# Kernel optimization log

Hardware: AMD Instinct MI355X
Metric: run time of the kernel (lower is better)

Reference implementation:

```python
import jax, jax.numpy as jnp
import numpy as np

B, S, V, D, H, C, NH = 8, 512, 32000, 768, 768, 9, 8
DH = D // NH


def setup_inputs() -> dict:
    key = jax.random.key(0)
    ks = list(jax.random.split(key, 24))
    it = iter(ks)

    def w(shape, s=0.02):
        return jax.random.normal(next(it), shape, jnp.float32) * s

    return {
        "input_ids": jax.random.randint(next(it), (B, S), 0, V, dtype=jnp.int32),
        "labels": jax.random.randint(next(it), (B, S), 0, C, dtype=jnp.int32),
        "emb_table": w((V, D), 1.0),
        "hw_Wh": w((D, D)),
        "hw_bh": jnp.zeros((D,), jnp.float32),
        "hw_Wt": w((D, D)),
        "hw_bt": jnp.zeros((D,), jnp.float32),
        "in_proj_w": w((3 * D, D)),
        "in_proj_b": jnp.zeros((3 * D,), jnp.float32),
        "out_proj_w": w((D, D)),
        "out_proj_b": jnp.zeros((D,), jnp.float32),
        "lstm0_Wih": w((2, 4 * H, D)),
        "lstm0_Whh": w((2, 4 * H, H)),
        "lstm0_b": jnp.zeros((2, 4 * H), jnp.float32),
        "lstm1_Wih": w((2, 4 * H, 2 * H)),
        "lstm1_Whh": w((2, 4 * H, H)),
        "lstm1_b": jnp.zeros((2, 4 * H), jnp.float32),
        "fc_W": w((C, 2 * H)),
        "fc_b": jnp.zeros((C,), jnp.float32),
        "crf_start": w((C,), 0.1),
        "crf_end": w((C,), 0.1),
        "crf_trans": w((C, C), 0.1),
    }


def _lstm_dir(x, Wih, Whh, b, reverse):
    # x: [B,S,in] -> outputs [B,S,H]; PyTorch gate order i,f,g,o
    xt = x.transpose(1, 0, 2)  # [S,B,in]
    h0 = jnp.zeros((x.shape[0], H), x.dtype)

    def step(carry, xt_):
        h, c = carry
        g = xt_ @ Wih.T + h @ Whh.T + b
        i, f, gg, o = jnp.split(g, 4, axis=-1)
        c = jax.nn.sigmoid(f) * c + jax.nn.sigmoid(i) * jnp.tanh(gg)
        h = jax.nn.sigmoid(o) * jnp.tanh(c)
        return (h, c), h

    _, hs = jax.lax.scan(step, (h0, h0), xt, reverse=reverse)
    return hs.transpose(1, 0, 2)


def _bilstm_layer(x, Wih, Whh, b):
    fwd = _lstm_dir(x, Wih[0], Whh[0], b[0], False)
    bwd = _lstm_dir(x, Wih[1], Whh[1], b[1], True)
    return jnp.concatenate([fwd, bwd], axis=-1)


def _emissions(input_ids, emb_table, hw_Wh, hw_bh, hw_Wt, hw_bt,
               in_proj_w, in_proj_b, out_proj_w, out_proj_b,
               lstm0_Wih, lstm0_Whh, lstm0_b, lstm1_Wih, lstm1_Whh, lstm1_b,
               fc_W, fc_b):
    x = emb_table[input_ids]  # [B,S,D]
    # Highway (1 layer, relu)
    hh = jax.nn.relu(x @ hw_Wh.T + hw_bh)
    t = jax.nn.sigmoid(x @ hw_Wt.T + hw_bt)
    x = t * hh + (1.0 - t) * x
    # Multi-head self-attention
    qkv = x @ in_proj_w.T + in_proj_b
    q, k, v = jnp.split(qkv, 3, axis=-1)
    hd = lambda a: a.reshape(B, S, NH, DH).transpose(0, 2, 1, 3)  # [B,NH,S,DH]
    q, k, v = hd(q), hd(k), hd(v)
    att = jax.nn.softmax(jnp.einsum('bhqd,bhkd->bhqk', q, k) / np.float32(np.sqrt(DH)), axis=-1)
    o = jnp.einsum('bhqk,bhkd->bhqd', att, v).transpose(0, 2, 1, 3).reshape(B, S, D)
    x = o @ out_proj_w.T + out_proj_b
    # 2-layer BiLSTM (inference: dropout off)
    x = _bilstm_layer(x, lstm0_Wih, lstm0_Whh, lstm0_b)
    x = _bilstm_layer(x, lstm1_Wih, lstm1_Whh, lstm1_b)
    return x @ fc_W.T + fc_b  # [B,S,C]


def _crf_nll(emissions, tags, crf_start, crf_end, crf_trans):
    # full mask (labels==-100 replaced by 0 before mask built), reduction='sum'
    em_t = emissions.transpose(1, 0, 2)  # [S,B,C]
    num = crf_start[tags[:, 0]] + crf_end[tags[:, -1]]
    num = num + jnp.take_along_axis(emissions, tags[..., None], axis=-1)[..., 0].sum(-1)
    num = num + crf_trans[tags[:, :-1], tags[:, 1:]].sum(-1)
    a0 = crf_start + em_t[0]  # [B,C]

    def fstep(a, em):
        a = jax.scipy.special.logsumexp(a[:, :, None] + crf_trans[None], axis=1) + em
        return a, None

    aT, _ = jax.lax.scan(fstep, a0, em_t[1:])
    logZ = jax.scipy.special.logsumexp(aT + crf_end, axis=-1)
    return -(num - logZ).sum()


def _viterbi(emissions, crf_start, crf_end, crf_trans):
    em_t = emissions.transpose(1, 0, 2)  # [S,B,C]
    s0 = crf_start + em_t[0]

    def vstep(s, em):
        sc = s[:, :, None] + crf_trans[None]  # [B,C_prev,C_next]
        return jnp.max(sc, axis=1) + em, jnp.argmax(sc, axis=1)

    sT, bps = jax.lax.scan(vstep, s0, em_t[1:])  # bps: [S-1,B,C]
    last = jnp.argmax(sT + crf_end, axis=-1)  # [B]

    def bstep(tag, bp):
        prev = jnp.take_along_axis(bp, tag[:, None], axis=1)[:, 0]
        return prev, prev

    _, path = jax.lax.scan(bstep, last, bps, reverse=True)  # [S-1,B]
    return jnp.concatenate([path, last[None]], axis=0).transpose(1, 0)  # [B,S]


def reference(input_ids, labels, emb_table, hw_Wh, hw_bh, hw_Wt, hw_bt,
              in_proj_w, in_proj_b, out_proj_w, out_proj_b,
              lstm0_Wih, lstm0_Whh, lstm0_b, lstm1_Wih, lstm1_Whh, lstm1_b,
              fc_W, fc_b, crf_start, crf_end, crf_trans):
    emissions = _emissions(input_ids, emb_table, hw_Wh, hw_bh, hw_Wt, hw_bt,
                           in_proj_w, in_proj_b, out_proj_w, out_proj_b,
                           lstm0_Wih, lstm0_Whh, lstm0_b,
                           lstm1_Wih, lstm1_Whh, lstm1_b, fc_W, fc_b)
    loss = _crf_nll(emissions, labels, crf_start, crf_end, crf_trans)
    decode = _viterbi(emissions, crf_start, crf_end, crf_trans)
    return loss, decode
```

## Files before the change

kernel.cpp:

```cpp
#include <hip/hip_runtime.h>
#include <cstdint>

#define B_   8
#define S_   512
#define D_   768
#define C_   9
#define BS_  4096

typedef unsigned long long u64;

__global__ __launch_bounds__(192) void k_embed(const int* __restrict__ ids,
                                               const float* __restrict__ emb,
                                               float* __restrict__ x) {
  int row = blockIdx.x;
  int id = ids[row];
  const float4* src = (const float4*)(emb + (size_t)id * D_);
  float4* dst = (float4*)(x + (size_t)row * D_);
  dst[threadIdx.x] = src[threadIdx.x];
}

#define GIDX(k, m) ((k)*144 + (m) + (((m) >> 5) << 2))

__global__ __launch_bounds__(256) void k_gemm(const float* __restrict__ A,
                                              const float* __restrict__ W,
                                              const float* __restrict__ bias,
                                              float* __restrict__ C,
                                              int M, int N, int K, int act, int mode) {
  __shared__ float As[2304];
  __shared__ float Bs[2304];
  int bm0 = blockIdx.y * 128, bn0 = blockIdx.x * 128;
  int tid = threadIdx.x;
  int tm = tid >> 4, tn = tid & 15;
  float acc[8][8];
#pragma unroll
  for (int i = 0; i < 8; ++i)
#pragma unroll
    for (int j = 0; j < 8; ++j) acc[i][j] = 0.f;

  for (int k0 = 0; k0 < K; k0 += 16) {
    __syncthreads();
#pragma unroll
    for (int j = 0; j < 2; ++j) {
      int f4 = tid + j * 256;
      int r = f4 >> 2;
      int kq = (f4 & 3) * 4;
      float4 va = *(const float4*)(A + (size_t)(bm0 + r) * K + k0 + kq);
      As[GIDX(kq + 0, r)] = va.x; As[GIDX(kq + 1, r)] = va.y;
      As[GIDX(kq + 2, r)] = va.z; As[GIDX(kq + 3, r)] = va.w;
      float4 vb = *(const float4*)(W + (size_t)(bn0 + r) * K + k0 + kq);
      Bs[GIDX(kq + 0, r)] = vb.x; Bs[GIDX(kq + 1, r)] = vb.y;
      Bs[GIDX(kq + 2, r)] = vb.z; Bs[GIDX(kq + 3, r)] = vb.w;
    }
    __syncthreads();
#pragma unroll
    for (int kk = 0; kk < 16; ++kk) {
      float a[8], b[8];
      *(float4*)&a[0] = *(const float4*)&As[GIDX(kk, tm * 8)];
      *(float4*)&a[4] = *(const float4*)&As[GIDX(kk, tm * 8 + 4)];
      *(float4*)&b[0] = *(const float4*)&Bs[GIDX(kk, tn * 8)];
      *(float4*)&b[4] = *(const float4*)&Bs[GIDX(kk, tn * 8 + 4)];
#pragma unroll
      for (int i = 0; i < 8; ++i)
#pragma unroll
        for (int j = 0; j < 8; ++j) acc[i][j] += a[i] * b[j];
    }
  }

  float bv[8];
#pragma unroll
  for (int j = 0; j < 8; ++j) bv[j] = bias[bn0 + tn * 8 + j];
#pragma unroll
  for (int i = 0; i < 8; ++i) {
    int row = bm0 + tm * 8 + i;
    float o[8];
#pragma unroll
    for (int j = 0; j < 8; ++j) {
      float v = acc[i][j] + bv[j];
      if (act == 1) v = fmaxf(v, 0.f);
      else if (act == 2) v = 1.f / (1.f + expf(-v));
      o[j] = v;
    }
    if (mode == 0) {
      float* cp = C + (size_t)row * N + bn0 + tn * 8;
      *(float4*)cp = make_float4(o[0], o[1], o[2], o[3]);
      *(float4*)(cp + 4) = make_float4(o[4], o[5], o[6], o[7]);
    } else {
      int bb = row >> 9, t = row & 511;
#pragma unroll
      for (int j = 0; j < 8; ++j) {
        unsigned n = bn0 + tn * 8 + j;
        unsigned dir = n / 3072u;
        unsigned n2 = n - dir * 3072u;
        unsigned g = n2 / 768u;
        unsigned rem = n2 - g * 768u;
        unsigned grp = rem >> 3, u = rem & 7;
        C[(((size_t)(dir * 512 + t) * 96 + grp) << 8) + u * 32 + g * 8 + bb] = o[j];
      }
    }
  }
}

__global__ __launch_bounds__(256) void k_highway(float* __restrict__ x,
                                                 const float* __restrict__ hh,
                                                 const float* __restrict__ tt) {
  const int n4 = BS_ * D_ / 4;
  for (int i = blockIdx.x * 256 + threadIdx.x; i < n4; i += gridDim.x * 256) {
    float4 xv = ((const float4*)x)[i];
    float4 hv = ((const float4*)hh)[i];
    float4 tv = ((const float4*)tt)[i];
    xv.x = tv.x * hv.x + (1.f - tv.x) * xv.x;
    xv.y = tv.y * hv.y + (1.f - tv.y) * xv.y;
    xv.z = tv.z * hv.z + (1.f - tv.z) * xv.z;
    xv.w = tv.w * hv.w + (1.f - tv.w) * xv.w;
    ((float4*)x)[i] = xv;
  }
}

__global__ __launch_bounds__(256) void k_attn(const float* __restrict__ qkv,
                                              float* __restrict__ out) {
  __shared__ float Qs[16 * 100];
  __shared__ float Ks[32 * 101];
  __shared__ float Ps[16 * 513];
  int bh = blockIdx.x;
  int b = bh >> 3, h = bh & 7;
  int q0 = blockIdx.y * 16;
  int tid = threadIdx.x;
  const float scale = 0.10206207261596577f;

  const float* qb = qkv + (size_t)(b * 512 + q0) * 2304 + h * 96;
  for (int i = tid; i < 16 * 96; i += 256) {
    int r = i / 96, c = i - r * 96;
    Qs[r * 100 + c] = qb[(size_t)r * 2304 + c];
  }
  int qi = tid >> 4, kseg = tid & 15;

  for (int kt = 0; kt < 16; ++kt) {
    __syncthreads();
    const float* kb = qkv + (size_t)(b * 512 + kt * 32) * 2304 + 768 + h * 96;
    for (int i = tid; i < 32 * 96; i += 256) {
      int r = i / 96, c = i - r * 96;
      Ks[r * 101 + c] = kb[(size_t)r * 2304 + c];
    }
    __syncthreads();
    int kj0 = kseg * 2;
    float s0 = 0.f, s1 = 0.f;
    const float* qrow = &Qs[qi * 100];
    const float* k0p = &Ks[kj0 * 101];
    const float* k1p = &Ks[(kj0 + 1) * 101];
#pragma unroll 8
    for (int d = 0; d < 96; ++d) {
      float qv = qrow[d];
      s0 += qv * k0p[d];
      s1 += qv * k1p[d];
    }
    Ps[qi * 513 + kt * 32 + kj0] = s0 * scale;
    Ps[qi * 513 + kt * 32 + kj0 + 1] = s1 * scale;
  }
  __syncthreads();

  {
    float m = -1e30f;
    for (int j = 0; j < 32; ++j) m = fmaxf(m, Ps[qi * 513 + kseg + j * 16]);
    m = fmaxf(m, __shfl_xor(m, 1)); m = fmaxf(m, __shfl_xor(m, 2));
    m = fmaxf(m, __shfl_xor(m, 4)); m = fmaxf(m, __shfl_xor(m, 8));
    float sum = 0.f;
    for (int j = 0; j < 32; ++j) {
      int idx = qi * 513 + kseg + j * 16;
      float e = expf(Ps[idx] - m);
      Ps[idx] = e;
      sum += e;
    }
    sum += __shfl_xor(sum, 1); sum += __shfl_xor(sum, 2);
    sum += __shfl_xor(sum, 4); sum += __shfl_xor(sum, 8);
    float inv = 1.f / sum;
    for (int j = 0; j < 32; ++j) Ps[qi * 513 + kseg + j * 16] *= inv;
  }

  float acc[6] = {0.f, 0.f, 0.f, 0.f, 0.f, 0.f};
  int d0 = kseg * 6;
  for (int kt = 0; kt < 16; ++kt) {
    __syncthreads();
    const float* vb = qkv + (size_t)(b * 512 + kt * 32) * 2304 + 1536 + h * 96;
    for (int i = tid; i < 32 * 96; i += 256) {
      int r = i / 96, c = i - r * 96;
      Ks[r * 101 + c] = vb[(size_t)r * 2304 + c];
    }
    __syncthreads();
#pragma unroll 4
    for (int kj = 0; kj < 32; ++kj) {
      float p = Ps[qi * 513 + kt * 32 + kj];
      const float* vrow = &Ks[kj * 101 + d0];
#pragma unroll
      for (int u = 0; u < 6; ++u) acc[u] += p * vrow[u];
    }
  }
  float* ob = out + (size_t)(b * 512 + q0 + qi) * 768 + h * 96 + d0;
#pragma unroll
  for (int u = 0; u < 6; ++u) ob[u] = acc[u];
}

#define NWGD 96
__global__ __launch_bounds__(256, 1) void k_lstm(const float* __restrict__ gates,
                                                 const float* __restrict__ Whh,
                                                 float* __restrict__ hbuf,
                                                 float* __restrict__ hs,
                                                 int* __restrict__ flags) {
  __shared__ float hlds[8 * 772];
  int tid = threadIdx.x;
  int wg = blockIdx.x;
  int dir = wg / NWGD;
  int grp = wg % NWGD;
  int rg = tid >> 5;
  int ks = tid & 31;

  float4 w4[4][6];
#pragma unroll
  for (int j = 0; j < 4; ++j) {
    const float* wp = Whh + ((size_t)dir * 3072 + j * 768 + grp * 8 + rg) * 768 + ks * 4;
#pragma unroll
    for (int jj = 0; jj < 6; ++jj)
      w4[j][jj] = *(const float4*)(wp + jj * 128);
  }

  float* hb = hbuf + (size_t)dir * 2 * 6144;
  const float* gbase = gates + (size_t)dir * 512 * 24576 + grp * 256 + tid;
  int* barp = flags;
  float cst = 0.f;
  const float* hp = hlds + ks * 4;

  for (int step = 0; step < 512; ++step) {
    int t = dir ? (511 - step) : step;
    float gqv = gbase[(size_t)t * 24576];

#pragma unroll
    for (int i = 0; i < 3; ++i) {
      int idx = i * 256 + tid;
      int b2 = idx / 96;
      int kq = (idx - b2 * 96) * 8;
      const u64* src = (const u64*)(hb + (step & 1) * 6144 + b2 * 768 + kq);
      u64 lo = __hip_atomic_load(src + 0, __ATOMIC_RELAXED, __HIP_MEMORY_SCOPE_AGENT);
      u64 hi = __hip_atomic_load(src + 1, __ATOMIC_RELAXED, __HIP_MEMORY_SCOPE_AGENT);
      u64 lo2 = __hip_atomic_load(src + 2, __ATOMIC_RELAXED, __HIP_MEMORY_SCOPE_AGENT);
      u64 hi2 = __hip_atomic_load(src + 3, __ATOMIC_RELAXED, __HIP_MEMORY_SCOPE_AGENT);
      float* dst = &hlds[b2 * 772 + kq];
      *(u64*)(dst + 0) = lo;
      *(u64*)(dst + 2) = hi;
      *(u64*)(dst + 4) = lo2;
      *(u64*)(dst + 6) = hi2;
    }
    __syncthreads();

    float v[32];
#pragma unroll
    for (int i = 0; i < 32; ++i) v[i] = 0.f;
#pragma unroll
    for (int jj = 0; jj < 6; ++jj) {
#pragma unroll
      for (int b2 = 0; b2 < 8; ++b2) {
        float4 hv = *(const float4*)(hp + b2 * 772 + jj * 128);
#pragma unroll
        for (int j = 0; j < 4; ++j) {
          float4 w = w4[j][jj];
          v[j * 8 + b2] = fmaf(w.x, hv.x, v[j * 8 + b2]);
          v[j * 8 + b2] = fmaf(w.y, hv.y, v[j * 8 + b2]);
          v[j * 8 + b2] = fmaf(w.z, hv.z, v[j * 8 + b2]);
          v[j * 8 + b2] = fmaf(w.w, hv.w, v[j * 8 + b2]);
        }
      }
    }

    {
      bool hi = (ks & 16) != 0;
#pragma unroll
      for (int i = 0; i < 16; ++i) {
        float keep = hi ? v[i + 16] : v[i];
        float send = hi ? v[i] : v[i + 16];
        v[i] = keep + __shfl_xor(send, 16);
      }
    }
    {
      bool hi = (ks & 8) != 0;
#pragma unroll
      for (int i = 0; i < 8; ++i) {
        float keep = hi ? v[i + 8] : v[i];
        float send = hi ? v[i] : v[i + 8];
        v[i] = keep + __shfl_xor(send, 8);
      }
    }
    {
      bool hi = (ks & 4) != 0;
#pragma unroll
      for (int i = 0; i < 4; ++i) {
        float keep = hi ? v[i + 4] : v[i];
        float send = hi ? v[i] : v[i + 4];
        v[i] = keep + __shfl_xor(send, 4);
      }
    }
    {
      bool hi = (ks & 2) != 0;
#pragma unroll
      for (int i = 0; i < 2; ++i) {
        float keep = hi ? v[i + 2] : v[i];
        float send = hi ? v[i] : v[i + 2];
        v[i] = keep + __shfl_xor(send, 2);
      }
    }
    {
      bool hi = (ks & 1) != 0;
      float keep = hi ? v[1] : v[0];
      float send = hi ? v[0] : v[1];
      v[0] = keep + __shfl_xor(send, 1);
    }

    float gv = v[0] + gqv;
    float gf = __shfl_down(gv, 8);
    float gg = __shfl_down(gv, 16);
    float go = __shfl_down(gv, 24);
    if (ks < 8) {
      float i_ = 1.f / (1.f + expf(-gv));
      float f_ = 1.f / (1.f + expf(-gf));
      float ci = tanhf(gg);
      float o_ = 1.f / (1.f + expf(-go));
      cst = f_ * cst + i_ * ci;
      float hnew = o_ * tanhf(cst);
      int hidden = grp * 8 + rg;
      __hip_atomic_store(hb + ((step + 1) & 1) * 6144 + ks * 768 + hidden, hnew,
                         __ATOMIC_RELAXED, __HIP_MEMORY_SCOPE_AGENT);
      hs[((size_t)(ks * 512 + t)) * 1536 + dir * 768 + hidden] = hnew;
    }

    __syncthreads();
    if (tid == 0)
      __hip_atomic_store(&barp[wg * 32], step + 1, __ATOMIC_RELAXED, __HIP_MEMORY_SCOPE_AGENT);
    if (tid < NWGD) {
      const int* fp = &barp[(dir * NWGD + tid) * 32];
      while (__hip_atomic_load(fp, __ATOMIC_RELAXED, __HIP_MEMORY_SCOPE_AGENT) <= step)
        __builtin_amdgcn_s_sleep(2);
    }
    __syncthreads();
  }
}

__global__ __launch_bounds__(256) void k_fc(const float* __restrict__ A,
                                            const float* __restrict__ Wf,
                                            const float* __restrict__ bf,
                                            float* __restrict__ out) {
  __shared__ float Wl[9 * 1536];
  int tid = threadIdx.x;
  for (int i = tid; i < 9 * 1536; i += 256) Wl[i] = Wf[i];
  __syncthreads();
  int lane = tid & 63, wv = tid >> 6;
  int row = blockIdx.x * 4 + wv;
  const float* a = A + (size_t)row * 1536;
  float acc[9];
#pragma unroll
  for (int c = 0; c < 9; ++c) acc[c] = 0.f;
  for (int i = 0; i < 24; ++i) {
    float av = a[lane + i * 64];
#pragma unroll
    for (int c = 0; c < 9; ++c) acc[c] += av * Wl[c * 1536 + lane + i * 64];
  }
#pragma unroll
  for (int c = 0; c < 9; ++c) {
#pragma unroll
    for (int m = 1; m < 64; m <<= 1) acc[c] += __shfl_xor(acc[c], m);
  }
  if (lane == 0) {
#pragma unroll
    for (int c = 0; c < 9; ++c) out[(size_t)row * 9 + c] = acc[c] + bf[c];
  }
}

__global__ __launch_bounds__(128) void k_crf(const float* __restrict__ em,
                                             const int* __restrict__ labels,
                                             const float* __restrict__ cs,
                                             const float* __restrict__ ce,
                                             const float* __restrict__ ct,
                                             float* __restrict__ out) {
  __shared__ float trans[9][12];
  __shared__ float ab[2][8][9];
  __shared__ float vb[2][8][9];
  __shared__ unsigned char bps[511][8][9];
  __shared__ float red[128];
  __shared__ float lz[8];
  int tid = threadIdx.x;
  if (tid < 81) trans[tid / 9][tid % 9] = ct[tid];
  if (tid < 72) {
    int b = tid / 9, c = tid % 9;
    float v = cs[c] + em[(b * 512) * 9 + c];
    ab[0][b][c] = v;
    vb[0][b][c] = v;
  }
  __syncthreads();
  for (int t = 1; t < 512; ++t) {
    int rp = (t - 1) & 1, wp = t & 1;
    if (tid < 72) {
      int b = tid / 9, cn = tid % 9;
      float e = em[(b * 512 + t) * 9 + cn];
      float m = -1e30f, vm = -1e30f;
      int bp = 0;
#pragma unroll
      for (int cp = 0; cp < 9; ++cp) {
        float x = ab[rp][b][cp] + trans[cp][cn];
        m = fmaxf(m, x);
        float y = vb[rp][b][cp] + trans[cp][cn];
        if (y > vm) { vm = y; bp = cp; }
      }
      float ssum = 0.f;
#pragma unroll
      for (int cp = 0; cp < 9; ++cp)
        ssum += expf(ab[rp][b][cp] + trans[cp][cn] - m);
      ab[wp][b][cn] = m + logf(ssum) + e;
      vb[wp][b][cn] = vm + e;
      bps[t - 1][b][cn] = (unsigned char)bp;
    }
    __syncthreads();
  }
  float part = 0.f;
  for (int idx = tid; idx < 4096; idx += 128) {
    int b = idx >> 9, t = idx & 511;
    int tg = labels[b * 512 + t];
    part += em[(b * 512 + t) * 9 + tg];
    if (t < 511) part += trans[tg][labels[b * 512 + t + 1]];
  }
  if (tid < 8) part += cs[labels[tid * 512]] + ce[labels[tid * 512 + 511]];
  red[tid] = part;
  __syncthreads();
  for (int s2 = 64; s2 > 0; s2 >>= 1) {
    if (tid < s2) red[tid] += red[tid + s2];
    __syncthreads();
  }
  if (tid < 8) {
    int b = tid;
    float m = -1e30f;
#pragma unroll
    for (int c = 0; c < 9; ++c) m = fmaxf(m, ab[1][b][c] + ce[c]);
    float ssum = 0.f;
#pragma unroll
    for (int c = 0; c < 9; ++c) ssum += expf(ab[1][b][c] + ce[c] - m);
    lz[b] = m + logf(ssum);
  }
  __syncthreads();
  if (tid == 0) {
    float z = 0.f;
#pragma unroll
    for (int b = 0; b < 8; ++b) z += lz[b];
    out[0] = -(red[0] - z);
  }
  if (tid < 8) {
    int b = tid;
    float bv2 = vb[1][b][0] + ce[0];
    int best = 0;
#pragma unroll
    for (int c = 1; c < 9; ++c) {
      float y = vb[1][b][c] + ce[c];
      if (y > bv2) { bv2 = y; best = c; }
    }
    out[1 + b * 512 + 511] = (float)best;
    int tg = best;
    for (int t = 510; t >= 0; --t) {
      tg = bps[t][b][tg];
      out[1 + b * 512 + t] = (float)tg;
    }
  }
}

extern "C" void kernel_launch(void* const* d_in, const int* in_sizes, int n_in,
                              void* d_out, int out_size, void* d_ws, size_t ws_size,
                              hipStream_t stream) {
  (void)in_sizes; (void)n_in; (void)out_size; (void)ws_size;
  const int*   ids    = (const int*)d_in[0];
  const int*   labels = (const int*)d_in[1];
  const float* emb    = (const float*)d_in[2];
  const float* hwWh   = (const float*)d_in[3];
  const float* hwbh   = (const float*)d_in[4];
  const float* hwWt   = (const float*)d_in[5];
  const float* hwbt   = (const float*)d_in[6];
  const float* ipw    = (const float*)d_in[7];
  const float* ipb    = (const float*)d_in[8];
  const float* opw    = (const float*)d_in[9];
  const float* opb    = (const float*)d_in[10];
  const float* l0Wih  = (const float*)d_in[11];
  const float* l0Whh  = (const float*)d_in[12];
  const float* l0b    = (const float*)d_in[13];
  const float* l1Wih  = (const float*)d_in[14];
  const float* l1Whh  = (const float*)d_in[15];
  const float* l1b    = (const float*)d_in[16];
  const float* fcW    = (const float*)d_in[17];
  const float* fcb    = (const float*)d_in[18];
  const float* cs     = (const float*)d_in[19];
  const float* ce     = (const float*)d_in[20];
  const float* ct     = (const float*)d_in[21];

  float* ws   = (float*)d_ws;
  float* x0   = ws;
  float* gbuf = ws + 3145728;
  float* hh   = gbuf;
  float* tt   = gbuf + 3145728;
  float* qkv  = gbuf + 6291456;
  float* x1   = ws + 28311552;
  float* hs0  = ws + 31457280;
  float* hs1  = ws + 37748736;
  float* em   = ws + 44040192;
  float* hbuf = ws + 44077056;
  int*   flags = (int*)(ws + 44101632);

  dim3 g768(6, 32), g2304(18, 32), g6144(48, 32);

  k_embed<<<BS_, 192, 0, stream>>>(ids, emb, x0);
  k_gemm<<<g768, 256, 0, stream>>>(x0, hwWh, hwbh, hh, BS_, 768, 768, 1, 0);
  k_gemm<<<g768, 256, 0, stream>>>(x0, hwWt, hwbt, tt, BS_, 768, 768, 2, 0);
  k_highway<<<768, 256, 0, stream>>>(x0, hh, tt);
  k_gemm<<<g2304, 256, 0, stream>>>(x0, ipw, ipb, qkv, BS_, 2304, 768, 0, 0);
  k_attn<<<dim3(64, 32), 256, 0, stream>>>(qkv, x0);
  k_gemm<<<g768, 256, 0, stream>>>(x0, opw, opb, x1, BS_, 768, 768, 0, 0);

  k_gemm<<<g6144, 256, 0, stream>>>(x1, l0Wih, l0b, gbuf, BS_, 6144, 768, 0, 1);
  hipMemsetAsync(hbuf, 0, (24576 + 192 * 32) * sizeof(float), stream);
  k_lstm<<<192, 256, 0, stream>>>(gbuf, l0Whh, hbuf, hs0, flags);

  k_gemm<<<g6144, 256, 0, stream>>>(hs0, l1Wih, l1b, gbuf, BS_, 6144, 1536, 0, 1);
  hipMemsetAsync(hbuf, 0, (24576 + 192 * 32) * sizeof(float), stream);
  k_lstm<<<192, 256, 0, stream>>>(gbuf, l1Whh, hbuf, hs1, flags);

  k_fc<<<1024, 256, 0, stream>>>(hs1, fcW, fcb, em);
  k_crf<<<1, 128, 0, stream>>>(em, labels, cs, ce, ct, (float*)d_out);
}
```

Baseline: 8.109 ms.

## Double-buffer GEMM smem, defer LSTM hs store, wave-per-batch CRF

The GEMM now uses double-buffered shared memory, with the next K-tile loaded into registers while the current one is computed, which removes one barrier per iteration. The LSTM step moves the global hs write after the barrier flag store so it leaves the critical path. The CRF kernel is rewritten to use one wavefront per batch, exchanging values with shuffles instead of a block-wide sync every timestep, and it prefetches emissions. The cost is more shared memory and registers in the GEMM, and a different CRF reduction order.

```diff
diff --git a/kernel.cpp b/kernel.cpp
--- a/kernel.cpp
+++ b/kernel.cpp
@@ -26,43 +26,69 @@
                                               const float* __restrict__ bias,
                                               float* __restrict__ C,
                                               int M, int N, int K, int act, int mode) {
-  __shared__ float As[2304];
-  __shared__ float Bs[2304];
+  __shared__ float As[2][2304];
+  __shared__ float Bs[2][2304];
   int bm0 = blockIdx.y * 128, bn0 = blockIdx.x * 128;
   int tid = threadIdx.x;
   int tm = tid >> 4, tn = tid & 15;
+  int r0 = tid >> 2, kq = (tid & 3) * 4;
+  const float* Aptr = A + (size_t)(bm0 + r0) * K + kq;
+  const float* Wptr = W + (size_t)(bn0 + r0) * K + kq;
+  const size_t rowK = (size_t)64 * K;
+
   float acc[8][8];
 #pragma unroll
   for (int i = 0; i < 8; ++i)
 #pragma unroll
     for (int j = 0; j < 8; ++j) acc[i][j] = 0.f;
 
+#define STAGE(buf, A0, A1, B0, B1)                                           \
+  {                                                                          \
+    As[buf][GIDX(kq + 0, r0)] = A0.x; As[buf][GIDX(kq + 1, r0)] = A0.y;      \
+    As[buf][GIDX(kq + 2, r0)] = A0.z; As[buf][GIDX(kq + 3, r0)] = A0.w;      \
+    As[buf][GIDX(kq + 0, r0 + 64)] = A1.x; As[buf][GIDX(kq + 1, r0 + 64)] = A1.y; \
+    As[buf][GIDX(kq + 2, r0 + 64)] = A1.z; As[buf][GIDX(kq + 3, r0 + 64)] = A1.w; \
+    Bs[buf][GIDX(kq + 0, r0)] = B0.x; Bs[buf][GIDX(kq + 1, r0)] = B0.y;      \
+    Bs[buf][GIDX(kq + 2, r0)] = B0.z; Bs[buf][GIDX(kq + 3, r0)] = B0.w;      \
+    Bs[buf][GIDX(kq + 0, r0 + 64)] = B1.x; Bs[buf][GIDX(kq + 1, r0 + 64)] = B1.y; \
+    Bs[buf][GIDX(kq + 2, r0 + 64)] = B1.z; Bs[buf][GIDX(kq + 3, r0 + 64)] = B1.w; \
+  }
+
+  {
+    float4 a0 = *(const float4*)(Aptr);
+    float4 a1 = *(const float4*)(Aptr + rowK);
+    float4 b0 = *(const float4*)(Wptr);
+    float4 b1 = *(const float4*)(Wptr + rowK);
+    STAGE(0, a0, a1, b0, b1);
+  }
+  __syncthreads();
+  int cur = 0;
+
   for (int k0 = 0; k0 < K; k0 += 16) {
-    __syncthreads();
-#pragma unroll
-    for (int j = 0; j < 2; ++j) {
-      int f4 = tid + j * 256;
-      int r = f4 >> 2;
-      int kq = (f4 & 3) * 4;
-      float4 va = *(const float4*)(A + (size_t)(bm0 + r) * K + k0 + kq);
-      As[GIDX(kq + 0, r)] = va.x; As[GIDX(kq + 1, r)] = va.y;
-      As[GIDX(kq + 2, r)] = va.z; As[GIDX(kq + 3, r)] = va.w;
-      float4 vb = *(const float4*)(W + (size_t)(bn0 + r) * K + k0 + kq);
-      Bs[GIDX(kq + 0, r)] = vb.x; Bs[GIDX(kq + 1, r)] = vb.y;
-      Bs[GIDX(kq + 2, r)] = vb.z; Bs[GIDX(kq + 3, r)] = vb.w;
-    }
-    __syncthreads();
+    bool more = (k0 + 16) < K;
+    float4 na0, na1, nb0, nb1;
+    if (more) {
+      na0 = *(const float4*)(Aptr + k0 + 16);
+      na1 = *(const float4*)(Aptr + rowK + k0 + 16);
+      nb0 = *(const float4*)(Wptr + k0 + 16);
+      nb1 = *(const float4*)(Wptr + rowK + k0 + 16);
+    }
 #pragma unroll
     for (int kk = 0; kk < 16; ++kk) {
       float a[8], b[8];
-      *(float4*)&a[0] = *(const float4*)&As[GIDX(kk, tm * 8)];
-      *(float4*)&a[4] = *(const float4*)&As[GIDX(kk, tm * 8 + 4)];
-      *(float4*)&b[0] = *(const float4*)&Bs[GIDX(kk, tn * 8)];
-      *(float4*)&b[4] = *(const float4*)&Bs[GIDX(kk, tn * 8 + 4)];
+      *(float4*)&a[0] = *(const float4*)&As[cur][GIDX(kk, tm * 8)];
+      *(float4*)&a[4] = *(const float4*)&As[cur][GIDX(kk, tm * 8 + 4)];
+      *(float4*)&b[0] = *(const float4*)&Bs[cur][GIDX(kk, tn * 8)];
+      *(float4*)&b[4] = *(const float4*)&Bs[cur][GIDX(kk, tn * 8 + 4)];
 #pragma unroll
       for (int i = 0; i < 8; ++i)
 #pragma unroll
         for (int j = 0; j < 8; ++j) acc[i][j] += a[i] * b[j];
+    }
+    if (more) {
+      STAGE(cur ^ 1, na0, na1, nb0, nb1);
+      __syncthreads();
+      cur ^= 1;
     }
   }
 
@@ -224,9 +250,8 @@
 
   float* hb = hbuf + (size_t)dir * 2 * 6144;
   const float* gbase = gates + (size_t)dir * 512 * 24576 + grp * 256 + tid;
-  int* barp = flags;
+  const float* hp = hlds + ks * 4;
   float cst = 0.f;
-  const float* hp = hlds + ks * 4;
 
   for (int step = 0; step < 512; ++step) {
     int t = dir ? (511 - step) : step;
@@ -238,8 +263,8 @@
       int b2 = idx / 96;
       int kq = (idx - b2 * 96) * 8;
       const u64* src = (const u64*)(hb + (step & 1) * 6144 + b2 * 768 + kq);
-      u64 lo = __hip_atomic_load(src + 0, __ATOMIC_RELAXED, __HIP_MEMORY_SCOPE_AGENT);
-      u64 hi = __hip_atomic_load(src + 1, __ATOMIC_RELAXED, __HIP_MEMORY_SCOPE_AGENT);
+      u64 lo  = __hip_atomic_load(src + 0, __ATOMIC_RELAXED, __HIP_MEMORY_SCOPE_AGENT);
+      u64 hi  = __hip_atomic_load(src + 1, __ATOMIC_RELAXED, __HIP_MEMORY_SCOPE_AGENT);
       u64 lo2 = __hip_atomic_load(src + 2, __ATOMIC_RELAXED, __HIP_MEMORY_SCOPE_AGENT);
       u64 hi2 = __hip_atomic_load(src + 3, __ATOMIC_RELAXED, __HIP_MEMORY_SCOPE_AGENT);
       float* dst = &hlds[b2 * 772 + kq];
@@ -316,24 +341,25 @@
     float gf = __shfl_down(gv, 8);
     float gg = __shfl_down(gv, 16);
     float go = __shfl_down(gv, 24);
+    float hnew = 0.f;
     if (ks < 8) {
       float i_ = 1.f / (1.f + expf(-gv));
       float f_ = 1.f / (1.f + expf(-gf));
       float ci = tanhf(gg);
       float o_ = 1.f / (1.f + expf(-go));
       cst = f_ * cst + i_ * ci;
-      float hnew = o_ * tanhf(cst);
-      int hidden = grp * 8 + rg;
-      __hip_atomic_store(hb + ((step + 1) & 1) * 6144 + ks * 768 + hidden, hnew,
-                         __ATOMIC_RELAXED, __HIP_MEMORY_SCOPE_AGENT);
-      hs[((size_t)(ks * 512 + t)) * 1536 + dir * 768 + hidden] = hnew;
+      hnew = o_ * tanhf(cst);
+      __hip_atomic_store(hb + (size_t)((step + 1) & 1) * 6144 + ks * 768 + grp * 8 + rg,
+                         hnew, __ATOMIC_RELAXED, __HIP_MEMORY_SCOPE_AGENT);
     }
 
     __syncthreads();
     if (tid == 0)
-      __hip_atomic_store(&barp[wg * 32], step + 1, __ATOMIC_RELAXED, __HIP_MEMORY_SCOPE_AGENT);
+      __hip_atomic_store(&flags[wg * 32], step + 1, __ATOMIC_RELAXED, __HIP_MEMORY_SCOPE_AGENT);
+    if (ks < 8)
+      hs[((size_t)(ks * 512 + t)) * 1536 + dir * 768 + grp * 8 + rg] = hnew;
     if (tid < NWGD) {
-      const int* fp = &barp[(dir * NWGD + tid) * 32];
+      const int* fp = &flags[(dir * NWGD + tid) * 32];
       while (__hip_atomic_load(fp, __ATOMIC_RELAXED, __HIP_MEMORY_SCOPE_AGENT) <= step)
         __builtin_amdgcn_s_sleep(2);
     }
@@ -371,97 +397,105 @@
   }
 }
 
-__global__ __launch_bounds__(128) void k_crf(const float* __restrict__ em,
+__global__ __launch_bounds__(512) void k_crf(const float* __restrict__ em,
                                              const int* __restrict__ labels,
                                              const float* __restrict__ cs,
                                              const float* __restrict__ ce,
                                              const float* __restrict__ ct,
                                              float* __restrict__ out) {
-  __shared__ float trans[9][12];
-  __shared__ float ab[2][8][9];
-  __shared__ float vb[2][8][9];
-  __shared__ unsigned char bps[511][8][9];
-  __shared__ float red[128];
-  __shared__ float lz[8];
+  __shared__ float trans_s[81];
+  __shared__ unsigned char bps[8][511][12];
+  __shared__ float partres[16];
   int tid = threadIdx.x;
-  if (tid < 81) trans[tid / 9][tid % 9] = ct[tid];
-  if (tid < 72) {
-    int b = tid / 9, c = tid % 9;
-    float v = cs[c] + em[(b * 512) * 9 + c];
-    ab[0][b][c] = v;
-    vb[0][b][c] = v;
-  }
+  int b = tid >> 6;
+  int lane = tid & 63;
+  bool act = lane < 9;
+  if (tid < 81) trans_s[tid] = ct[tid];
   __syncthreads();
+
+  float tcol[9];
+#pragma unroll
+  for (int cp = 0; cp < 9; ++cp) tcol[cp] = act ? trans_s[cp * 9 + lane] : 0.f;
+
+  float a_ = -1e30f, v_ = -1e30f;
+  if (act) {
+    float e0 = em[((size_t)b * 512) * 9 + lane];
+    a_ = cs[lane] + e0;
+    v_ = a_;
+  }
+
+  float e = act ? em[((size_t)b * 512 + 1) * 9 + lane] : 0.f;
   for (int t = 1; t < 512; ++t) {
-    int rp = (t - 1) & 1, wp = t & 1;
-    if (tid < 72) {
-      int b = tid / 9, cn = tid % 9;
-      float e = em[(b * 512 + t) * 9 + cn];
-      float m = -1e30f, vm = -1e30f;
-      int bp = 0;
-#pragma unroll
-      for (int cp = 0; cp < 9; ++cp) {
-        float x = ab[rp][b][cp] + trans[cp][cn];
-        m = fmaxf(m, x);
-        float y = vb[rp][b][cp] + trans[cp][cn];
-        if (y > vm) { vm = y; bp = cp; }
-      }
-      float ssum = 0.f;
-#pragma unroll
-      for (int cp = 0; cp < 9; ++cp)
-        ssum += expf(ab[rp][b][cp] + trans[cp][cn] - m);
-      ab[wp][b][cn] = m + logf(ssum) + e;
-      vb[wp][b][cn] = vm + e;
-      bps[t - 1][b][cn] = (unsigned char)bp;
-    }
-    __syncthreads();
-  }
-  float part = 0.f;
-  for (int idx = tid; idx < 4096; idx += 128) {
-    int b = idx >> 9, t = idx & 511;
+    float e_nxt = 0.f;
+    if (act && t < 511) e_nxt = em[((size_t)b * 512 + t + 1) * 9 + lane];
+    float m = -1e30f, vm = -1e30f;
+    int bp = 0;
+    float xs[9];
+#pragma unroll
+    for (int cp = 0; cp < 9; ++cp) {
+      float ap = __shfl(a_, cp);
+      float vp = __shfl(v_, cp);
+      float x = ap + tcol[cp];
+      xs[cp] = x;
+      m = fmaxf(m, x);
+      float y = vp + tcol[cp];
+      if (y > vm) { vm = y; bp = cp; }
+    }
+    float ssum = 0.f;
+#pragma unroll
+    for (int cp = 0; cp < 9; ++cp) ssum += expf(xs[cp] - m);
+    if (act) {
+      a_ = m + logf(ssum) + e;
+      v_ = vm + e;
+      bps[b][t - 1][lane] = (unsigned char)bp;
+    }
+    e = e_nxt;
+  }
+
+  float fin = act ? a_ + ce[lane] : -1e30f;
+  float vfin = act ? v_ + ce[lane] : -1e30f;
+  float m2 = fin;
+  m2 = fmaxf(m2, __shfl_xor(m2, 1)); m2 = fmaxf(m2, __shfl_xor(m2, 2));
+  m2 = fmaxf(m2, __shfl_xor(m2, 4)); m2 = fmaxf(m2, __shfl_xor(m2, 8));
+  float s2 = expf(fin - m2);
+  s2 += __shfl_xor(s2, 1); s2 += __shfl_xor(s2, 2);
+  s2 += __shfl_xor(s2, 4); s2 += __shfl_xor(s2, 8);
+  float logZ = m2 + logf(s2);
+
+  float bv = vfin; int bi = lane;
+#pragma unroll
+  for (int s = 1; s < 16; s <<= 1) {
+    float ov = __shfl_xor(bv, s);
+    int oi = __shfl_xor(bi, s);
+    if (ov > bv || (ov == bv && oi < bi)) { bv = ov; bi = oi; }
+  }
+
+  float np = 0.f;
+  for (int t = lane; t < 512; t += 64) {
     int tg = labels[b * 512 + t];
-    part += em[(b * 512 + t) * 9 + tg];
-    if (t < 511) part += trans[tg][labels[b * 512 + t + 1]];
-  }
-  if (tid < 8) part += cs[labels[tid * 512]] + ce[labels[tid * 512 + 511]];
-  red[tid] = part;
-  __syncthreads();
-  for (int s2 = 64; s2 > 0; s2 >>= 1) {
-    if (tid < s2) red[tid] += red[tid + s2];
-    __syncthreads();
-  }
-  if (tid < 8) {
-    int b = tid;
-    float m = -1e30f;
-#pragma unroll
-    for (int c = 0; c < 9; ++c) m = fmaxf(m, ab[1][b][c] + ce[c]);
-    float ssum = 0.f;
-#pragma unroll
-    for (int c = 0; c < 9; ++c) ssum += expf(ab[1][b][c] + ce[c] - m);
-    lz[b] = m + logf(ssum);
+    np += em[((size_t)b * 512 + t) * 9 + tg];
+    if (t < 511) np += trans_s[tg * 9 + labels[b * 512 + t + 1]];
+  }
+#pragma unroll
+  for (int s = 1; s < 64; s <<= 1) np += __shfl_xor(np, s);
+
+  if (lane == 0) {
+    np += cs[labels[b * 512]] + ce[labels[b * 512 + 511]];
+    partres[b] = np;
+    partres[8 + b] = logZ;
+    out[1 + b * 512 + 511] = (float)bi;
+    int tg = bi;
+    for (int t = 510; t >= 0; --t) {
+      tg = bps[b][t][tg];
+      out[1 + b * 512 + t] = (float)tg;
+    }
   }
   __syncthreads();
   if (tid == 0) {
-    float z = 0.f;
-#pragma unroll
-    for (int b = 0; b < 8; ++b) z += lz[b];
-    out[0] = -(red[0] - z);
-  }
-  if (tid < 8) {
-    int b = tid;
-    float bv2 = vb[1][b][0] + ce[0];
-    int best = 0;
-#pragma unroll
-    for (int c = 1; c < 9; ++c) {
-      float y = vb[1][b][c] + ce[c];
-      if (y > bv2) { bv2 = y; best = c; }
-    }
-    out[1 + b * 512 + 511] = (float)best;
-    int tg = best;
-    for (int t = 510; t >= 0; --t) {
-      tg = bps[t][b][tg];
-      out[1 + b * 512 + t] = (float)tg;
-    }
+    float acc = 0.f;
+#pragma unroll
+    for (int b2 = 0; b2 < 8; ++b2) acc += partres[b2] - partres[8 + b2];
+    out[0] = -acc;
   }
 }
 
@@ -524,5 +558,5 @@
   k_lstm<<<192, 256, 0, stream>>>(gbuf, l1Whh, hbuf, hs1, flags);
 
   k_fc<<<1024, 256, 0, stream>>>(hs1, fcW, fcb, em);
-  k_crf<<<1, 128, 0, stream>>>(em, labels, cs, ce, ct, (float*)d_out);
-}
+  k_crf<<<1, 512, 0, stream>>>(em, labels, cs, ce, ct, (float*)d_out);
+}
```

Result: no change. 8.152 ms (+0.5%).
